# Kernel optimization log

Measured on AMD Instinct MI355X. Metric: run time of the kernel, lower is better.

Reference implementation:

```python
import jax, jax.numpy as jnp
import numpy as np

B, S, E, H = 4, 2048, 1024, 16
D = E // H


def setup_inputs() -> dict:
    key = jax.random.key(0)
    ks = jax.random.split(key, 6)
    scale = 1.0 / np.sqrt(E).astype(np.float32)
    return {
        "x": jax.random.normal(ks[0], (B, S, E), jnp.float32),
        # positive entries -> cumsum normalizer is well conditioned
        "weight": jax.random.uniform(ks[1], (H, S), jnp.float32, 0.05, 1.0),
        "bias": jax.random.normal(ks[2], (H, S), jnp.float32) * 0.02,
        "inp_w": jax.random.normal(ks[3], (E, E), jnp.float32) * scale,
        "inp_b": jax.random.normal(ks[4], (E,), jnp.float32) * 0.02,
        "out_w": jax.random.normal(ks[5], (E, E), jnp.float32) * scale,
    }


def reference(x, weight, bias, inp_w, inp_b, out_w):
    Bx, Sx, Ex = x.shape
    Hx = weight.shape[0]
    Dx = Ex // Hx
    # input projection (torch Linear: x @ W.T + b)
    x = x @ inp_w.T + inp_b
    # (B,S,E) -> (B,E,S) -> (B,H,D,S)
    xh = x.transpose(0, 2, 1).reshape(Bx, Hx, Dx, Sx)
    # Toeplitz causal matrix per head: M[h,i,j] = weight[h, j-i] if j>=i else 0
    idx = jnp.arange(Sx)
    off = idx[None, :] - idx[:, None]  # (S,S)
    M = jnp.where(off >= 0, weight[:, off], jnp.zeros((), x.dtype))  # (H,S,S)
    # batched matmul over the sequence axis: y[b,h,d,t] = sum_s x[b,h,d,s] M[h,s,t]
    y = jnp.einsum('bhds,hst->bhdt', xh, M)
    # cumulative-sum normalization (do_toep_mean=True)
    norm = jnp.cumsum(weight, axis=-1)  # (H,S)
    y = y / norm[None, :, None, :]
    # per-head, per-position bias
    y = y + bias[None, :, None, :]
    # (B,H,D,S) -> (B,E,S) -> (B,S,E)
    y = y.reshape(Bx, Ex, Sx).transpose(0, 2, 1)
    # output projection (no bias)
    return y @ out_w.T
```

## Files before the change

### kernel.cpp

```cpp
#include <hip/hip_runtime.h>

typedef unsigned short u16;
typedef __attribute__((ext_vector_type(4))) float f32x4;
typedef __attribute__((ext_vector_type(8))) __bf16 bf16x8;

__device__ __forceinline__ u16 f2bf(float f) {
  unsigned u = __builtin_bit_cast(unsigned, f);
  u = u + 0x7fffu + ((u >> 16) & 1u);
  return (u16)(u >> 16);
}

__device__ __forceinline__ void load_lds16(const void* g, void* l) {
  __builtin_amdgcn_global_load_lds((__attribute__((address_space(1))) void*)g,
                                   (__attribute__((address_space(3))) void*)l,
                                   16, 0, 0);
}

__device__ __forceinline__ f32x4 MF(bf16x8 a, bf16x8 b, f32x4 c) {
  return __builtin_amdgcn_mfma_f32_16x16x32_bf16(a, b, c, 0, 0, 0);
}

__global__ __launch_bounds__(256) void prep_pre(const float* __restrict__ x,
                                                const float* __restrict__ inp_w,
                                                u16* __restrict__ Xb,
                                                u16* __restrict__ Wb) {
  const int bx = blockIdx.x, tid = threadIdx.x;
  const float* src; u16* dst; int i;
  if (bx < 8192) { src = x;     dst = Xb; i = bx * 256 + tid; }
  else           { src = inp_w; dst = Wb; i = (bx - 8192) * 256 + tid; }
  const float4 v = ((const float4*)src)[i];
  ushort4 o;
  o.x = f2bf(v.x); o.y = f2bf(v.y); o.z = f2bf(v.z); o.w = f2bf(v.w);
  ((ushort4*)dst)[i] = o;
}

__device__ void prep_post_block(int ex, int tid,
                                const float* __restrict__ out_w,
                                const float* __restrict__ weight,
                                u16* __restrict__ OWb,
                                float* __restrict__ normB,
                                u16* __restrict__ V) {
  if (ex < 1024) {
    const int i = ex * 256 + tid;
    const float4 v = ((const float4*)out_w)[i];
    ushort4 o;
    o.x = f2bf(v.x); o.y = f2bf(v.y); o.z = f2bf(v.z); o.w = f2bf(v.w);
    ((ushort4*)OWb)[i] = o;
    return;
  }
  if (ex < 1040) {
    const int h = ex - 1024;
    __shared__ float ts[256];
    float v[8];
    const float* src = weight + h * 2048 + tid * 8;
    float s = 0.f;
#pragma unroll
    for (int j = 0; j < 8; ++j) v[j] = src[j];
#pragma unroll
    for (int j = 0; j < 8; ++j) { s += v[j]; v[j] = s; }
    ts[tid] = s;
    __syncthreads();
    float xx = s;
#pragma unroll
    for (int d = 1; d < 256; d <<= 1) {
      float y = (tid >= d) ? ts[tid - d] : 0.f;
      __syncthreads();
      xx += y;
      ts[tid] = xx;
      __syncthreads();
    }
    const float excl = xx - s;
    float* dst = normB + h * 2048 + tid * 8;
#pragma unroll
    for (int j = 0; j < 8; ++j) dst[j] = excl + v[j];
    return;
  }
  {
    const int bb = ex - 1040;
    const int h = bb & 15, tb = bb >> 4;
    __shared__ u16 wl[2048];
#pragma unroll
    for (int j = 0; j < 8; ++j) wl[tid * 8 + j] = f2bf(weight[h * 2048 + tid * 8 + j]);
    __syncthreads();
#pragma unroll
    for (int i = 0; i < 8; ++i) {
      const int cid = i * 256 + tid;
      const int row = cid >> 4, c = cid & 15;
      const int t = tb * 128 + row;
      const int j0 = c * 8;
      unsigned v[8];
#pragma unroll
      for (int jj = 0; jj < 8; ++jj) {
        const int j = j0 + jj;
        v[jj] = (t >= j) ? (unsigned)wl[t - j] : 0u;
      }
      uint4 o;
      o.x = v[0] | (v[1] << 16); o.y = v[2] | (v[3] << 16);
      o.z = v[4] | (v[5] << 16); o.w = v[6] | (v[7] << 16);
      *(uint4*)(V + ((size_t)(h * 2048 + t)) * 128 + j0) = o;
    }
  }
}

template <bool BIAS, bool F32OUT, int DEC, bool POST>
__global__ __launch_bounds__(256) void gemm_nt4(const u16* __restrict__ A,
                                                const u16* __restrict__ B,
                                                void* __restrict__ C,
                                                const float* __restrict__ bias,
                                                int K, int lda, int ldb, int ldc,
                                                const float* __restrict__ out_w,
                                                const float* __restrict__ weight,
                                                u16* __restrict__ OWb,
                                                float* __restrict__ normB,
                                                u16* __restrict__ Vt) {
  const int flatAll = (int)blockIdx.x;
  if (POST && flatAll >= 512) {
    prep_post_block(flatAll - 512, threadIdx.x, out_w, weight, OWb, normB, Vt);
    return;
  }
  __shared__ __align__(16) u16 As[2][128 * 64];
  __shared__ __align__(16) u16 Bs[2][128 * 64];
  const int tid = threadIdx.x;
  const int lane = tid & 63, wv = tid >> 6;
  const int wm = wv >> 1, wn = wv & 1;
  const int l15 = lane & 15, g = lane >> 4;

  const int flat = flatAll;
  int m0, n0;
  if (DEC == 0) {
    const int xcd = flat & 7, i = flat >> 3;
    m0 = (i & 7) * 128;
    n0 = ((xcd << 3) + (i >> 3)) * 128;
  } else {
    const int sw = (flat & 7) * 64 + (flat >> 3);
    m0 = (sw >> 3) * 128;
    n0 = (sw & 7) * 128;
  }

  const int NT = K >> 6;

  auto stage = [&](int t, int bi) {
    const int kt = t << 6;
#pragma unroll
    for (int i = 0; i < 4; ++i) {
      const int c = i * 256 + tid;
      const int row = c >> 3, cc = c & 7;
      load_lds16(A + (size_t)(m0 + row) * lda + kt + ((cc ^ (row & 7)) << 3),
                 &As[bi][i * 2048 + wv * 512]);
    }
#pragma unroll
    for (int i = 0; i < 4; ++i) {
      const int c = i * 256 + tid;
      const int row = c >> 3, cc = c & 7;
      load_lds16(B + (size_t)(n0 + row) * ldb + kt + ((cc ^ (row & 7)) << 3),
                 &Bs[bi][i * 2048 + wv * 512]);
    }
  };

  f32x4 acc[4][4] = {};
  stage(0, 0);
  __syncthreads();
  int cur = 0;
  for (int t = 0; t < NT; ++t) {
    if (t + 1 < NT) stage(t + 1, cur ^ 1);
#pragma unroll
    for (int kh = 0; kh < 2; ++kh) {
      bf16x8 af[4], bf[4];
#pragma unroll
      for (int mf = 0; mf < 4; ++mf) {
        const int row = wm * 64 + mf * 16 + l15;
        af[mf] = *(const bf16x8*)(&As[cur][row * 64 + ((((kh << 2) + g) ^ (row & 7)) << 3)]);
      }
#pragma unroll
      for (int nf = 0; nf < 4; ++nf) {
        const int row = wn * 64 + nf * 16 + l15;
        bf[nf] = *(const bf16x8*)(&Bs[cur][row * 64 + ((((kh << 2) + g) ^ (row & 7)) << 3)]);
      }
      __builtin_amdgcn_s_setprio(1);
#pragma unroll
      for (int mf = 0; mf < 4; ++mf)
#pragma unroll
        for (int nf = 0; nf < 4; ++nf)
          acc[mf][nf] = MF(af[mf], bf[nf], acc[mf][nf]);
      __builtin_amdgcn_s_setprio(0);
    }
    __syncthreads();
    cur ^= 1;
  }

#pragma unroll
  for (int mf = 0; mf < 4; ++mf) {
#pragma unroll
    for (int r = 0; r < 4; ++r) {
      const int row = m0 + wm * 64 + mf * 16 + g * 4 + r;
      const float bb = BIAS ? bias[row] : 0.f;
#pragma unroll
      for (int nf = 0; nf < 4; ++nf) {
        const int col = n0 + wn * 64 + nf * 16 + l15;
        const float v = acc[mf][nf][r] + bb;
        if (F32OUT)
          ((float*)C)[(size_t)row * ldc + col] = v;
        else
          ((u16*)C)[(size_t)row * ldc + col] = f2bf(v);
      }
    }
  }
}

__global__ __launch_bounds__(256) void toep_conv(const u16* __restrict__ X1t,
                                                 const u16* __restrict__ V,
                                                 const float* __restrict__ normB,
                                                 const float* __restrict__ biasB,
                                                 u16* __restrict__ Y2b) {
  __shared__ __align__(16) u16 As[3][128 * 64];
  __shared__ __align__(16) u16 Xs[3][64 * 64];
  const int tid = threadIdx.x;
  const int lane = tid & 63, wv = tid >> 6;
  const int l15 = lane & 15, g = lane >> 4;

  const int x = (int)blockIdx.x;
  const int h = (x & 7) + 8 * ((x >> 3) & 1);
  const int pb = x >> 4;
  const int pair = pb & 7, b = pb >> 3;

  const u16* Vh = V + (size_t)h * 2048 * 128;
  const u16* Xrow = X1t + (size_t)h * 64 * 8192 + b * 2048;

#pragma unroll 1
  for (int ti = 0; ti < 2; ++ti) {
    const int tt = ti ? pair : 15 - pair;
    const int t0 = tt * 128;
    const int Q = (tt + 1) * 2;
    f32x4 acc[2][4] = {};

    auto stage = [&](int q, int bufi) {
      const int st = q >> 1, k = q & 1;
      const int s0 = st * 128 + k * 64;
#pragma unroll
      for (int i = 0; i < 2; ++i) {
        const int c = i * 256 + tid;
        const int row = c >> 3, cc = c & 7;
        load_lds16(Xrow + (size_t)row * 8192 + s0 + ((cc ^ (row & 7)) * 8),
                   &Xs[bufi][i * 2048 + wv * 512]);
      }
      const u16* Ab = Vh + (size_t)(tt - st) * 128 * 128 + k * 64;
#pragma unroll
      for (int i = 0; i < 4; ++i) {
        const int c = i * 256 + tid;
        const int row = c >> 3, cc = c & 7;
        load_lds16(Ab + row * 128 + ((cc ^ (row & 7)) * 8),
                   &As[bufi][i * 2048 + wv * 512]);
      }
    };

    stage(0, 0);
    if (Q > 1) stage(1, 1);
    asm volatile("s_waitcnt vmcnt(6)" ::: "memory");
    __builtin_amdgcn_sched_barrier(0);
    __builtin_amdgcn_s_barrier();
    asm volatile("" ::: "memory");

    int cur = 0;
    for (int q = 0; q < Q; ++q) {
      if (q + 2 < Q) stage(q + 2, (q + 2) % 3);
#pragma unroll
      for (int ks = 0; ks < 2; ++ks) {
        bf16x8 af[2];
#pragma unroll
        for (int tf = 0; tf < 2; ++tf) {
          const int row = wv * 32 + tf * 16 + l15;
          af[tf] = *(const bf16x8*)(&As[cur][row * 64 + (((ks * 4 + g) ^ (row & 7)) * 8)]);
        }
        __builtin_amdgcn_s_setprio(1);
#pragma unroll
        for (int nf = 0; nf < 4; ++nf) {
          const int row = nf * 16 + l15;
          const bf16x8 bv = *(const bf16x8*)(&Xs[cur][row * 64 + (((ks * 4 + g) ^ (row & 7)) * 8)]);
#pragma unroll
          for (int tf = 0; tf < 2; ++tf)
            acc[tf][nf] = MF(af[tf], bv, acc[tf][nf]);
        }
        __builtin_amdgcn_s_setprio(0);
      }
      if (q + 2 < Q)      asm volatile("s_waitcnt vmcnt(6)" ::: "memory");
      else if (q + 1 < Q) asm volatile("s_waitcnt vmcnt(0)" ::: "memory");
      __builtin_amdgcn_sched_barrier(0);
      __builtin_amdgcn_s_barrier();
      asm volatile("" ::: "memory");
      cur = (cur == 2) ? 0 : cur + 1;
    }

#pragma unroll
    for (int tf = 0; tf < 2; ++tf) {
#pragma unroll
      for (int r = 0; r < 4; ++r) {
        const int t = t0 + wv * 32 + tf * 16 + g * 4 + r;
        const float inv = 1.0f / normB[h * 2048 + t];
        const float bb = biasB[h * 2048 + t];
#pragma unroll
        for (int nf = 0; nf < 4; ++nf) {
          const int d = nf * 16 + l15;
          Y2b[(size_t)(b * 2048 + t) * 1024 + h * 64 + d] = f2bf(acc[tf][nf][r] * inv + bb);
        }
      }
    }
  }
}

extern "C" void kernel_launch(void* const* d_in, const int* in_sizes, int n_in,
                              void* d_out, int out_size, void* d_ws, size_t ws_size,
                              hipStream_t stream) {
  (void)in_sizes; (void)n_in; (void)out_size; (void)ws_size;
  const float* x      = (const float*)d_in[0];
  const float* weight = (const float*)d_in[1];
  const float* biasB  = (const float*)d_in[2];
  const float* inp_w  = (const float*)d_in[3];
  const float* inp_b  = (const float*)d_in[4];
  const float* out_w  = (const float*)d_in[5];

  char* ws = (char*)d_ws;
  u16* Xb    = (u16*)(ws + 0);
  u16* X1t   = (u16*)(ws + (size_t)(16u << 20));
  u16* Y2b   = (u16*)(ws + (size_t)(32u << 20));
  u16* Wb    = (u16*)(ws + (size_t)(48u << 20));
  u16* OWb   = (u16*)(ws + (size_t)(50u << 20));
  float* normB = (float*)(ws + (size_t)(53u << 20));
  u16* Vt    = (u16*)(ws + (size_t)(56u << 20));

  prep_pre<<<9216, 256, 0, stream>>>(x, inp_w, Xb, Wb);

  gemm_nt4<true, false, 0, true><<<1808, 256, 0, stream>>>(
      Wb, Xb, (void*)X1t, inp_b, 1024, 1024, 1024, 8192,
      out_w, weight, OWb, normB, Vt);

  toep_conv<<<512, 256, 0, stream>>>(X1t, Vt, normB, biasB, Y2b);

  gemm_nt4<false, true, 1, false><<<512, 256, 0, stream>>>(
      Y2b, OWb, d_out, nullptr, 1024, 1024, 1024, 1024,
      nullptr, nullptr, nullptr, nullptr, nullptr);
}
```

Before: 96.20 us.

## Fuse fp32-to-bf16 conversion of x into the input projection GEMM

The separate pass that converts the 8M-element x tensor to bf16 is dropped. The input-projection GEMM now loads fp32 x tiles into registers, converts them to bf16 and writes them into LDS, while A tiles still arrive through async global-to-LDS loads in a triple buffer. This removes one full write and one full read of a bf16 copy of x. In exchange the GEMM reads twice the bytes for B through the register path, and the manual barrier/waitcnt pipeline adds register pressure and some risk of synchronisation hazards.

```diff
diff --git a/kernel.cpp b/kernel.cpp
--- a/kernel.cpp
+++ b/kernel.cpp
@@ -2,6 +2,7 @@
 
 typedef unsigned short u16;
 typedef __attribute__((ext_vector_type(4))) float f32x4;
+typedef __attribute__((ext_vector_type(8))) short short8;
 typedef __attribute__((ext_vector_type(8))) __bf16 bf16x8;
 
 __device__ __forceinline__ u16 f2bf(float f) {
@@ -20,18 +21,13 @@
   return __builtin_amdgcn_mfma_f32_16x16x32_bf16(a, b, c, 0, 0, 0);
 }
 
-__global__ __launch_bounds__(256) void prep_pre(const float* __restrict__ x,
-                                                const float* __restrict__ inp_w,
-                                                u16* __restrict__ Xb,
+__global__ __launch_bounds__(256) void prep_pre(const float* __restrict__ inp_w,
                                                 u16* __restrict__ Wb) {
-  const int bx = blockIdx.x, tid = threadIdx.x;
-  const float* src; u16* dst; int i;
-  if (bx < 8192) { src = x;     dst = Xb; i = bx * 256 + tid; }
-  else           { src = inp_w; dst = Wb; i = (bx - 8192) * 256 + tid; }
-  const float4 v = ((const float4*)src)[i];
+  const int i = blockIdx.x * 256 + threadIdx.x;
+  const float4 v = ((const float4*)inp_w)[i];
   ushort4 o;
   o.x = f2bf(v.x); o.y = f2bf(v.y); o.z = f2bf(v.z); o.w = f2bf(v.w);
-  ((ushort4*)dst)[i] = o;
+  ((ushort4*)Wb)[i] = o;
 }
 
 __device__ void prep_post_block(int ex, int tid,
@@ -102,22 +98,131 @@
   }
 }
 
-template <bool BIAS, bool F32OUT, int DEC, bool POST>
+__global__ __launch_bounds__(256) void gemm_bf32(const u16* __restrict__ A,
+                                                 const float* __restrict__ Bf,
+                                                 u16* __restrict__ C,
+                                                 const float* __restrict__ bias,
+                                                 const float* __restrict__ out_w,
+                                                 const float* __restrict__ weight,
+                                                 u16* __restrict__ OWb,
+                                                 float* __restrict__ normB,
+                                                 u16* __restrict__ Vt) {
+  const int flatAll = (int)blockIdx.x;
+  if (flatAll >= 512) {
+    prep_post_block(flatAll - 512, threadIdx.x, out_w, weight, OWb, normB, Vt);
+    return;
+  }
+  __shared__ __align__(16) u16 As[3][128 * 64];
+  __shared__ __align__(16) u16 Bs[2][128 * 64];
+  const int tid = threadIdx.x;
+  const int lane = tid & 63, wv = tid >> 6;
+  const int wm = wv >> 1, wn = wv & 1;
+  const int l15 = lane & 15, g = lane >> 4;
+
+  const int xcd = flatAll & 7, bi_ = flatAll >> 3;
+  const int m0 = (bi_ & 7) * 128;
+  const int n0 = ((xcd << 3) + (bi_ >> 3)) * 128;
+
+  const int NT = 16;
+  const int srow = tid >> 3, scc = tid & 7;
+
+  auto stageA = [&](int t, int bi) {
+    const int kt = t << 6;
+#pragma unroll
+    for (int i = 0; i < 4; ++i) {
+      const int c = i * 256 + tid;
+      const int row = c >> 3, cc = c & 7;
+      load_lds16(A + (size_t)(m0 + row) * 1024 + kt + ((cc ^ (row & 7)) << 3),
+                 &As[bi][i * 2048 + wv * 512]);
+    }
+  };
+
+  float4 br[8];
+  auto loadBreg = [&](int t) {
+    const int kt = t << 6;
+#pragma unroll
+    for (int i = 0; i < 4; ++i) {
+      const int row = (i * 256 + tid) >> 3, cc = (i * 256 + tid) & 7;
+      const float* p = Bf + (size_t)(n0 + row) * 1024 + kt + cc * 8;
+      br[2 * i]     = *(const float4*)(p);
+      br[2 * i + 1] = *(const float4*)(p + 4);
+    }
+  };
+  auto writeB = [&](int bi) {
+#pragma unroll
+    for (int i = 0; i < 4; ++i) {
+      const int row = (i * 256 + tid) >> 3, cc = (i * 256 + tid) & 7;
+      short8 v;
+      v[0] = (short)f2bf(br[2 * i].x);     v[1] = (short)f2bf(br[2 * i].y);
+      v[2] = (short)f2bf(br[2 * i].z);     v[3] = (short)f2bf(br[2 * i].w);
+      v[4] = (short)f2bf(br[2 * i + 1].x); v[5] = (short)f2bf(br[2 * i + 1].y);
+      v[6] = (short)f2bf(br[2 * i + 1].z); v[7] = (short)f2bf(br[2 * i + 1].w);
+      *(short8*)(&Bs[bi][row * 64 + ((cc ^ (row & 7)) << 3)]) = v;
+    }
+  };
+
+  f32x4 acc[4][4] = {};
+  stageA(0, 0);
+  loadBreg(0);
+
+#pragma unroll 1
+  for (int t = 0; t < NT; ++t) {
+    writeB(t & 1);
+    if (t + 1 < NT) {
+      stageA(t + 1, (t + 1) % 3);
+      loadBreg(t + 1);
+    }
+    asm volatile("s_waitcnt lgkmcnt(0)" ::: "memory");
+    __builtin_amdgcn_sched_barrier(0);
+    __builtin_amdgcn_s_barrier();
+    __builtin_amdgcn_sched_barrier(0);
+
+    const u16* Ac = &As[t % 3][0];
+    const u16* Bc = &Bs[t & 1][0];
+#pragma unroll
+    for (int kh = 0; kh < 2; ++kh) {
+      bf16x8 af[4], bf[4];
+#pragma unroll
+      for (int mf = 0; mf < 4; ++mf) {
+        const int row = wm * 64 + mf * 16 + l15;
+        af[mf] = *(const bf16x8*)(Ac + row * 64 + ((((kh << 2) + g) ^ (row & 7)) << 3));
+      }
+#pragma unroll
+      for (int nf = 0; nf < 4; ++nf) {
+        const int row = wn * 64 + nf * 16 + l15;
+        bf[nf] = *(const bf16x8*)(Bc + row * 64 + ((((kh << 2) + g) ^ (row & 7)) << 3));
+      }
+      __builtin_amdgcn_s_setprio(1);
+#pragma unroll
+      for (int mf = 0; mf < 4; ++mf)
+#pragma unroll
+        for (int nf = 0; nf < 4; ++nf)
+          acc[mf][nf] = MF(af[mf], bf[nf], acc[mf][nf]);
+      __builtin_amdgcn_s_setprio(0);
+    }
+    __builtin_amdgcn_s_barrier();
+  }
+
+#pragma unroll
+  for (int mf = 0; mf < 4; ++mf) {
+#pragma unroll
+    for (int r = 0; r < 4; ++r) {
+      const int row = m0 + wm * 64 + mf * 16 + g * 4 + r;
+      const float bb = bias[row];
+#pragma unroll
+      for (int nf = 0; nf < 4; ++nf) {
+        const int col = n0 + wn * 64 + nf * 16 + l15;
+        C[(size_t)row * 8192 + col] = f2bf(acc[mf][nf][r] + bb);
+      }
+    }
+  }
+  (void)srow; (void)scc;
+}
+
 __global__ __launch_bounds__(256) void gemm_nt4(const u16* __restrict__ A,
                                                 const u16* __restrict__ B,
-                                                void* __restrict__ C,
-                                                const float* __restrict__ bias,
-                                                int K, int lda, int ldb, int ldc,
-                                                const float* __restrict__ out_w,
-                                                const float* __restrict__ weight,
-                                                u16* __restrict__ OWb,
-                                                float* __restrict__ normB,
-                                                u16* __restrict__ Vt) {
-  const int flatAll = (int)blockIdx.x;
-  if (POST && flatAll >= 512) {
-    prep_post_block(flatAll - 512, threadIdx.x, out_w, weight, OWb, normB, Vt);
-    return;
-  }
+                                                float* __restrict__ C,
+                                                int K, int lda, int ldb, int ldc) {
   __shared__ __align__(16) u16 As[2][128 * 64];
   __shared__ __align__(16) u16 Bs[2][128 * 64];
   const int tid = threadIdx.x;
@@ -125,17 +230,10 @@
   const int wm = wv >> 1, wn = wv & 1;
   const int l15 = lane & 15, g = lane >> 4;
 
-  const int flat = flatAll;
-  int m0, n0;
-  if (DEC == 0) {
-    const int xcd = flat & 7, i = flat >> 3;
-    m0 = (i & 7) * 128;
-    n0 = ((xcd << 3) + (i >> 3)) * 128;
-  } else {
-    const int sw = (flat & 7) * 64 + (flat >> 3);
-    m0 = (sw >> 3) * 128;
-    n0 = (sw & 7) * 128;
-  }
+  const int flat = (int)blockIdx.x;
+  const int sw = (flat & 7) * 64 + (flat >> 3);
+  const int m0 = (sw >> 3) * 128;
+  const int n0 = (sw & 7) * 128;
 
   const int NT = K >> 6;
 
@@ -193,15 +291,10 @@
 #pragma unroll
     for (int r = 0; r < 4; ++r) {
       const int row = m0 + wm * 64 + mf * 16 + g * 4 + r;
-      const float bb = BIAS ? bias[row] : 0.f;
 #pragma unroll
       for (int nf = 0; nf < 4; ++nf) {
         const int col = n0 + wn * 64 + nf * 16 + l15;
-        const float v = acc[mf][nf][r] + bb;
-        if (F32OUT)
-          ((float*)C)[(size_t)row * ldc + col] = v;
-        else
-          ((u16*)C)[(size_t)row * ldc + col] = f2bf(v);
+        C[(size_t)row * ldc + col] = acc[mf][nf][r];
       }
     }
   }
@@ -319,7 +412,6 @@
   const float* out_w  = (const float*)d_in[5];
 
   char* ws = (char*)d_ws;
-  u16* Xb    = (u16*)(ws + 0);
   u16* X1t   = (u16*)(ws + (size_t)(16u << 20));
   u16* Y2b   = (u16*)(ws + (size_t)(32u << 20));
   u16* Wb    = (u16*)(ws + (size_t)(48u << 20));
@@ -327,15 +419,12 @@
   float* normB = (float*)(ws + (size_t)(53u << 20));
   u16* Vt    = (u16*)(ws + (size_t)(56u << 20));
 
-  prep_pre<<<9216, 256, 0, stream>>>(x, inp_w, Xb, Wb);
-
-  gemm_nt4<true, false, 0, true><<<1808, 256, 0, stream>>>(
-      Wb, Xb, (void*)X1t, inp_b, 1024, 1024, 1024, 8192,
-      out_w, weight, OWb, normB, Vt);
+  prep_pre<<<1024, 256, 0, stream>>>(inp_w, Wb);
+
+  gemm_bf32<<<1808, 256, 0, stream>>>(Wb, x, X1t, inp_b,
+                                      out_w, weight, OWb, normB, Vt);
 
   toep_conv<<<512, 256, 0, stream>>>(X1t, Vt, normB, biasB, Y2b);
 
-  gemm_nt4<false, true, 1, false><<<512, 256, 0, stream>>>(
-      Y2b, OWb, d_out, nullptr, 1024, 1024, 1024, 1024,
-      nullptr, nullptr, nullptr, nullptr, nullptr);
-}
+  gemm_nt4<<<512, 256, 0, stream>>>(Y2b, OWb, (float*)d_out, 1024, 1024, 1024, 1024);
+}
```

After: 123.3 us. +28.1%, slower.
